# Optimization experiments

Measured on AMD Instinct MI355X. Metric: run time of the kernel, lower is better.

The kernel has to match this reference:

```python
import jax, jax.numpy as jnp
import numpy as np

T, N, D, E, O = 2, 4096, 1024, 8, 1024

def setup_inputs() -> dict:
    key = jax.random.key(0)
    k1, k2, k3 = jax.random.split(key, 3)
    x = jax.random.normal(k1, (T, N, D), dtype=jnp.float32)
    Wg = jax.random.normal(k2, (T, D, E), dtype=jnp.float32) * (1.0 / np.sqrt(D))
    We = jax.random.normal(k3, (E, D, O), dtype=jnp.float32) * (1.0 / np.sqrt(D))
    return {"x": x, "Wg": Wg, "We": We, "k": 2}


def reference(x, Wg, We, k):
    # Per-task gating logits: [T, N, E]
    logits = jnp.einsum('tnd,tde->tne', x, Wg)
    # Top-k mask per token (scatter 1.0 at top-k indices)
    _, topk_idx = jax.lax.top_k(logits, k)                      # [T, N, k]
    mask = jax.nn.one_hot(topk_idx, E, dtype=logits.dtype).sum(-2)  # [T, N, E]
    masked = mask * logits
    gates = masked / (masked.sum(-1, keepdims=True) + 1e-9)     # [T, N, E]
    # Dense expert outputs (each expert is Linear(D, O)): [T, N, E, O]
    eout = jnp.einsum('tnd,edo->tneo', x, We)
    # Weighted combine over selected experts
    out = jnp.einsum('tne,tneo->tno', gates, eout)              # [T, N, O]
    return out
```

## Files before the change

kernel.cpp:

```cpp
#include <hip/hip_runtime.h>
#include <hip/hip_bf16.h>
#include <stdint.h>

#define T_ 2
#define N_ 4096
#define D_ 1024
#define E_ 8
#define O_ 1024

#define BM 128
#define BN 128
#define BK 32

typedef __attribute__((ext_vector_type(8))) short short8;
typedef __attribute__((ext_vector_type(4))) float f32x4;

#define AS1 __attribute__((address_space(1)))
#define AS3 __attribute__((address_space(3)))

__device__ inline void gld16(const unsigned short* g, unsigned short* l) {
    __builtin_amdgcn_global_load_lds((const AS1 unsigned int*)g,
                                     (AS3 unsigned int*)l, 16, 0, 0);
}

__device__ inline unsigned short f2bf(float f) {
    union { float f; unsigned u; } v; v.f = f;
    unsigned r = v.u + 0x7fff + ((v.u >> 16) & 1);
    return (unsigned short)(r >> 16);
}

__global__ __launch_bounds__(256) void gate_kernel(
    const float* __restrict__ x, const float* __restrict__ Wg,
    unsigned short* __restrict__ xb,
    int* __restrict__ route, float2* __restrict__ gpair)
{
    __shared__ __align__(16) float WgT[E_][D_];

    int tid = threadIdx.x;
    int wave = tid >> 6, lane = tid & 63;
    int token0 = blockIdx.x * 16;
    int t = token0 >> 12;
    const float* wgb = Wg + (size_t)t * D_ * E_;

#pragma unroll
    for (int r = 0; r < 8; ++r) {
        int f = r * 1024 + tid * 4;
        float4 v = *(const float4*)(wgb + f);
        WgT[f & 7][f >> 3]             = v.x;
        WgT[(f + 1) & 7][(f + 1) >> 3] = v.y;
        WgT[(f + 2) & 7][(f + 2) >> 3] = v.z;
        WgT[(f + 3) & 7][(f + 3) >> 3] = v.w;
    }
    __syncthreads();

    for (int tl = 0; tl < 4; ++tl) {
        int token = token0 + wave * 4 + tl;
        const float* xrow = x + (size_t)token * D_;

        float4 xv[4];
#pragma unroll
        for (int c = 0; c < 4; ++c)
            xv[c] = *(const float4*)(xrow + c * 256 + lane * 4);

        float acc[E_] = {0.f, 0.f, 0.f, 0.f, 0.f, 0.f, 0.f, 0.f};
#pragma unroll
        for (int c = 0; c < 4; ++c) {
            int d0 = c * 256 + lane * 4;
            unsigned lo = f2bf(xv[c].x) | ((unsigned)f2bf(xv[c].y) << 16);
            unsigned hi = f2bf(xv[c].z) | ((unsigned)f2bf(xv[c].w) << 16);
            *(uint2*)(&xb[(size_t)token * D_ + d0]) = make_uint2(lo, hi);
#pragma unroll
            for (int e = 0; e < E_; ++e) {
                float4 w = *(const float4*)(&WgT[e][d0]);
                acc[e] += xv[c].x * w.x + xv[c].y * w.y + xv[c].z * w.z + xv[c].w * w.w;
            }
        }
#pragma unroll
        for (int off = 1; off < 64; off <<= 1) {
#pragma unroll
            for (int e = 0; e < E_; ++e) acc[e] += __shfl_xor(acc[e], off, 64);
        }

        if (lane == 0) {
            float best = acc[0]; int bi = 0;
#pragma unroll
            for (int e = 1; e < E_; ++e) if (acc[e] > best) { best = acc[e]; bi = e; }
            float sec = -INFINITY; int si = 0;
#pragma unroll
            for (int e = 0; e < E_; ++e) if (e != bi && acc[e] > sec) { sec = acc[e]; si = e; }
            float s = best + sec + 1e-9f;
            route[token] = bi | (si << 8);
            gpair[token] = make_float2(best / s, sec / s);
        }
    }
}

__global__ __launch_bounds__(256) void build_lists(
    const int* __restrict__ route, const float2* __restrict__ gpair,
    int* __restrict__ toklist, float* __restrict__ gatelist,
    int* __restrict__ counts)
{
    int g = blockIdx.x;
    int t = g >> 3, e = g & 7;
    int tid = threadIdx.x;
    int wave = tid >> 6, lane = tid & 63;

    __shared__ int waveSum[4];
    __shared__ int base;
    if (tid == 0) base = 0;

    for (int c = 0; c < N_; c += 256) {
        int n = c + tid;
        int r = route[t * N_ + n];
        int e0 = r & 255, e1 = (r >> 8) & 255;
        bool sel = (e0 == e) || (e1 == e);
        unsigned long long b = __ballot(sel);
        int pre  = __popcll(b & ((1ull << lane) - 1ull));
        if (lane == 0) waveSum[wave] = __popcll(b);
        __syncthreads();
        int woff = 0;
#pragma unroll
        for (int w = 0; w < 4; ++w) woff += (w < wave) ? waveSum[w] : 0;
        int total = waveSum[0] + waveSum[1] + waveSum[2] + waveSum[3];
        if (sel) {
            int p = base + woff + pre;
            toklist[g * N_ + p] = n;
            float2 gp = gpair[t * N_ + n];
            gatelist[g * N_ + p] = (e0 == e) ? gp.x : gp.y;
        }
        __syncthreads();
        if (tid == 0) base += total;
    }
    __syncthreads();
    if (tid == 0) counts[g] = base;
}

__global__ __launch_bounds__(256) void pack_kernel(
    const float* __restrict__ We, unsigned short* __restrict__ Wbp)
{
    __shared__ __align__(16) unsigned short P[64 * 136];

    int b = blockIdx.x;
    int e  = b >> 7;
    int oy = (b & 127) >> 3;
    int dz = b & 7;
    int o0 = oy * 64, d0 = dz * 128;
    int tid = threadIdx.x;

#pragma unroll
    for (int r = 0; r < 32; ++r) {
        int lin = r * 256 + tid;
        int dd = lin >> 6, oo = lin & 63;
        P[oo * 136 + dd] = f2bf(We[((size_t)(e * D_ + d0 + dd)) * O_ + o0 + oo]);
    }
    __syncthreads();

#pragma unroll
    for (int w = 0; w < 4; ++w) {
        int ci = w * 256 + tid;
        int oo = ci >> 4, dc = ci & 15;
        uint4 v = *(const uint4*)&P[oo * 136 + dc * 8];
        int o = o0 + oo;
        int ot = o >> 7, nn = o & 127;
        unsigned short* dst =
            Wbp + ((size_t)((e * 8 + ot) * 128 + nn)) * D_ + d0 + dc * 8;
        *(uint4*)dst = v;
    }
}

__global__ __launch_bounds__(256) void moe_gemm(
    const unsigned short* __restrict__ xb,
    const unsigned short* __restrict__ Wbp,
    const int* __restrict__ toklist, const float* __restrict__ gatelist,
    const int* __restrict__ counts, float* __restrict__ out)
{
    int lin = blockIdx.x + (blockIdx.y << 5) + (blockIdx.z << 8);
    int xcd = lin & 7, slot = lin >> 3;
    int mt = slot & 31;
    int pr = xcd * 16 + (slot >> 5);
    int ot = pr & 7;
    int g  = pr >> 3;
    int t  = g >> 3;

    int cnt = counts[g];
    int m0 = mt * BM;
    if (m0 >= cnt) return;

    __shared__ __align__(16) unsigned short As[BM * 32];
    __shared__ __align__(16) unsigned short Bs[BN * 32];
    __shared__ int   tokS[BM];
    __shared__ float gateS[BM];

    int tid = threadIdx.x;
    if (tid < BM) {
        int r = m0 + tid;
        tokS[tid]  = (r < cnt) ? toklist[g * N_ + r]  : -1;
        gateS[tid] = (r < cnt) ? gatelist[g * N_ + r] : 0.f;
    }
    __syncthreads();

    int wave = tid >> 6, lane = tid & 63;
    int lr = lane >> 2;
    int lc = (lane & 3) * 8;
    int c0 = wave * 2, c1 = c0 + 1;
    int ar0 = c0 * 16 + lr, ar1 = c1 * 16 + lr;
    int tok0 = max(tokS[ar0], 0), tok1 = max(tokS[ar1], 0);
    const unsigned short* ag0 = xb + ((size_t)(t * N_ + tok0)) * D_ + lc;
    const unsigned short* ag1 = xb + ((size_t)(t * N_ + tok1)) * D_ + lc;
    const unsigned short* wb  = Wbp + ((size_t)((g & 7) * 8 + ot) * 128) * D_;
    const unsigned short* bg0 = wb + (size_t)ar0 * D_ + lc;
    const unsigned short* bg1 = wb + (size_t)ar1 * D_ + lc;
    unsigned short* la0 = &As[c0 * 16 * 32];
    unsigned short* la1 = &As[c1 * 16 * 32];
    unsigned short* lb0 = &Bs[c0 * 16 * 32];
    unsigned short* lb1 = &Bs[c1 * 16 * 32];

    int wm = (wave & 1) * 64, wn = (wave >> 1) * 64;
    int fr = lane & 15, q = lane >> 4;

    f32x4 acc[4][4];
#pragma unroll
    for (int mi = 0; mi < 4; ++mi)
#pragma unroll
        for (int ni = 0; ni < 4; ++ni) acc[mi][ni] = (f32x4){0.f, 0.f, 0.f, 0.f};

    for (int k0 = 0; k0 < D_; k0 += BK) {
        gld16(ag0 + k0, la0);
        gld16(ag1 + k0, la1);
        gld16(bg0 + k0, lb0);
        gld16(bg1 + k0, lb1);
        __syncthreads();

        short8 af[4], bf[4];
#pragma unroll
        for (int mi = 0; mi < 4; ++mi)
            af[mi] = *(const short8*)(&As[(wm + mi * 16 + fr) * 32 + q * 8]);
#pragma unroll
        for (int ni = 0; ni < 4; ++ni)
            bf[ni] = *(const short8*)(&Bs[(wn + ni * 16 + fr) * 32 + q * 8]);
#pragma unroll
        for (int mi = 0; mi < 4; ++mi)
#pragma unroll
            for (int ni = 0; ni < 4; ++ni)
                acc[mi][ni] = __builtin_amdgcn_mfma_f32_16x16x32_bf16(
                    af[mi], bf[ni], acc[mi][ni], 0, 0, 0);
        __syncthreads();
    }

    float* outb = out + (size_t)t * N_ * O_;
    int ncol = ot * 128 + wn + fr;
#pragma unroll
    for (int mi = 0; mi < 4; ++mi) {
#pragma unroll
        for (int r = 0; r < 4; ++r) {
            int ml = wm + mi * 16 + q * 4 + r;
            int tok = tokS[ml];
            if (tok >= 0) {
                float gate = gateS[ml];
#pragma unroll
                for (int ni = 0; ni < 4; ++ni)
                    atomicAdd(&outb[(size_t)tok * O_ + ncol + ni * 16],
                              gate * acc[mi][ni][r]);
            }
        }
    }
}

extern "C" void kernel_launch(void* const* d_in, const int* in_sizes, int n_in,
                              void* d_out, int out_size, void* d_ws, size_t ws_size,
                              hipStream_t stream)
{
    const float* x  = (const float*)d_in[0];
    const float* Wg = (const float*)d_in[1];
    const float* We = (const float*)d_in[2];
    float* out = (float*)d_out;

    char* ws = (char*)d_ws;
    unsigned short* xb   = (unsigned short*)(ws);
    unsigned short* Wbp  = (unsigned short*)(ws + 16777216);
    int*   toklist       = (int*)  (ws + 33554432);
    float* gatelist      = (float*)(ws + 33816576);
    int*   counts        = (int*)  (ws + 34078720);
    int*   route         = (int*)  (ws + 34078976);
    float2* gpair        = (float2*)(ws + 34111744);

    hipMemsetAsync(out, 0, (size_t)T_ * N_ * O_ * sizeof(float), stream);

    gate_kernel<<<(T_ * N_) / 16, 256, 0, stream>>>(x, Wg, xb, route, gpair);
    build_lists<<<T_ * E_, 256, 0, stream>>>(route, gpair, toklist, gatelist, counts);
    pack_kernel<<<E_ * (O_ / 64) * (D_ / 128), 256, 0, stream>>>(We, Wbp);
    moe_gemm<<<dim3(N_ / BM, O_ / BN, T_ * E_), 256, 0, stream>>>(
        xb, Wbp, toklist, gatelist, counts, out);
}
```

Before: 218.0 us.

## Replace output atomics with per-slot bf16 halves and a combine pass

Each token's two expert contributions are now stored as bf16 values in the low and high halves of its fp32 output word, instead of being added with fp32 atomicAdd. The expert's slot index is packed into bit 16 of the token list entry. A new combine kernel then sums the two halves into fp32, which also removes the output memset. The gate kernel now handles 32 tokens per block instead of 16. The aim is to drop atomic traffic and the zero-fill, at the cost of an extra full pass over the output and bf16 rounding of each partial result.

```diff
diff --git a/kernel.cpp b/kernel.cpp
--- a/kernel.cpp
+++ b/kernel.cpp
@@ -38,7 +38,7 @@
 
     int tid = threadIdx.x;
     int wave = tid >> 6, lane = tid & 63;
-    int token0 = blockIdx.x * 16;
+    int token0 = blockIdx.x * 32;
     int t = token0 >> 12;
     const float* wgb = Wg + (size_t)t * D_ * E_;
 
@@ -53,8 +53,8 @@
     }
     __syncthreads();
 
-    for (int tl = 0; tl < 4; ++tl) {
-        int token = token0 + wave * 4 + tl;
+    for (int tl = 0; tl < 8; ++tl) {
+        int token = token0 + wave * 8 + tl;
         const float* xrow = x + (size_t)token * D_;
 
         float4 xv[4];
@@ -124,7 +124,8 @@
         int total = waveSum[0] + waveSum[1] + waveSum[2] + waveSum[3];
         if (sel) {
             int p = base + woff + pre;
-            toklist[g * N_ + p] = n;
+            int slot = (e0 == e) ? 0 : 1;
+            toklist[g * N_ + p] = n | (slot << 16);
             float2 gp = gpair[t * N_ + n];
             gatelist[g * N_ + p] = (e0 == e) ? gp.x : gp.y;
         }
@@ -175,9 +176,9 @@
     const int* __restrict__ counts, float* __restrict__ out)
 {
     int lin = blockIdx.x + (blockIdx.y << 5) + (blockIdx.z << 8);
-    int xcd = lin & 7, slot = lin >> 3;
-    int mt = slot & 31;
-    int pr = xcd * 16 + (slot >> 5);
+    int xcd = lin & 7, slot_ = lin >> 3;
+    int mt = slot_ & 31;
+    int pr = xcd * 16 + (slot_ >> 5);
     int ot = pr & 7;
     int g  = pr >> 3;
     int t  = g >> 3;
@@ -204,7 +205,8 @@
     int lc = (lane & 3) * 8;
     int c0 = wave * 2, c1 = c0 + 1;
     int ar0 = c0 * 16 + lr, ar1 = c1 * 16 + lr;
-    int tok0 = max(tokS[ar0], 0), tok1 = max(tokS[ar1], 0);
+    int tok0 = max(tokS[ar0], 0) & 0xFFFF;
+    int tok1 = max(tokS[ar1], 0) & 0xFFFF;
     const unsigned short* ag0 = xb + ((size_t)(t * N_ + tok0)) * D_ + lc;
     const unsigned short* ag1 = xb + ((size_t)(t * N_ + tok1)) * D_ + lc;
     const unsigned short* wb  = Wbp + ((size_t)((g & 7) * 8 + ot) * 128) * D_;
@@ -254,16 +256,33 @@
 #pragma unroll
         for (int r = 0; r < 4; ++r) {
             int ml = wm + mi * 16 + q * 4 + r;
-            int tok = tokS[ml];
-            if (tok >= 0) {
+            int ent = tokS[ml];
+            if (ent >= 0) {
+                int tok  = ent & 0xFFFF;
+                int slot = ent >> 16;
                 float gate = gateS[ml];
 #pragma unroll
-                for (int ni = 0; ni < 4; ++ni)
-                    atomicAdd(&outb[(size_t)tok * O_ + ncol + ni * 16],
-                              gate * acc[mi][ni][r]);
+                for (int ni = 0; ni < 4; ++ni) {
+                    unsigned short* p =
+                        (unsigned short*)(outb + (size_t)tok * O_ + ncol + ni * 16);
+                    p[slot] = f2bf(gate * acc[mi][ni][r]);
+                }
             }
         }
     }
+}
+
+__global__ __launch_bounds__(256) void combine_kernel(float* __restrict__ out)
+{
+    size_t i = ((size_t)blockIdx.x * 256 + threadIdx.x) * 4;
+    unsigned* po = (unsigned*)out;
+    uint4 v = *(uint4*)(po + i);
+    float4 r;
+    union { unsigned u; float f; } a, b;
+#define CMB(comp, src) a.u = (src) << 16; b.u = (src) & 0xFFFF0000u; comp = a.f + b.f
+    CMB(r.x, v.x); CMB(r.y, v.y); CMB(r.z, v.z); CMB(r.w, v.w);
+#undef CMB
+    *(float4*)(out + i) = r;
 }
 
 extern "C" void kernel_launch(void* const* d_in, const int* in_sizes, int n_in,
@@ -284,11 +303,10 @@
     int*   route         = (int*)  (ws + 34078976);
     float2* gpair        = (float2*)(ws + 34111744);
 
-    hipMemsetAsync(out, 0, (size_t)T_ * N_ * O_ * sizeof(float), stream);
-
-    gate_kernel<<<(T_ * N_) / 16, 256, 0, stream>>>(x, Wg, xb, route, gpair);
+    gate_kernel<<<(T_ * N_) / 32, 256, 0, stream>>>(x, Wg, xb, route, gpair);
     build_lists<<<T_ * E_, 256, 0, stream>>>(route, gpair, toklist, gatelist, counts);
     pack_kernel<<<E_ * (O_ / 64) * (D_ / 128), 256, 0, stream>>>(We, Wbp);
     moe_gemm<<<dim3(N_ / BM, O_ / BN, T_ * E_), 256, 0, stream>>>(
         xb, Wbp, toklist, gatelist, counts, out);
-}
+    combine_kernel<<<((size_t)T_ * N_ * O_) / (256 * 4), 256, 0, stream>>>(out);
+}
```

After: 203.2 us. 6.8% less time.
